# Kernel optimization log

Hardware: AMD Instinct MI355X
Metric: run time of the kernel (lower is better)

Reference implementation:

```python
import jax, jax.numpy as jnp
import numpy as np

N_NODES = 100000
N_EDGES = 3200000
IN_F = 128
HEADS = 8
OUT_C = 2  # GATConv out_channels hardcoded to 2 in the source
NEG_SLOPE = 0.2  # PyG GATConv default leaky_relu slope


def setup_inputs() -> dict:
    key = jax.random.key(0)
    ks = jax.random.split(key, 9)
    x = jax.random.normal(ks[0], (N_NODES, IN_F), dtype=jnp.float32)
    edge_index = jax.random.randint(ks[1], (2, N_EDGES), 0, N_NODES, dtype=jnp.int64)
    edge_attr = jax.random.uniform(ks[2], (N_EDGES, 1), dtype=jnp.float32)
    s = 1.0 / np.sqrt(IN_F)
    W = jax.random.normal(ks[3], (IN_F, HEADS * OUT_C), dtype=jnp.float32) * s
    att_src = jax.random.normal(ks[4], (HEADS, OUT_C), dtype=jnp.float32) * 0.5
    att_dst = jax.random.normal(ks[5], (HEADS, OUT_C), dtype=jnp.float32) * 0.5
    bias_gat = jnp.zeros((HEADS * OUT_C,), dtype=jnp.float32)
    W_fc = jax.random.normal(ks[6], (HEADS * OUT_C, 2), dtype=jnp.float32) * 0.25
    b_fc = jnp.zeros((2,), dtype=jnp.float32)
    return {"x": x, "edge_index": edge_index, "edge_attr": edge_attr,
            "W": W, "att_src": att_src, "att_dst": att_dst,
            "bias_gat": bias_gat, "W_fc": W_fc, "b_fc": b_fc}


def reference(x, edge_index, edge_attr, W, att_src, att_dst, bias_gat, W_fc, b_fc):
    # edge_attr is ignored: GATConv was built without edge_dim, matching the source.
    N = x.shape[0]
    # PyG GATConv adds self-loops by default
    loops = jnp.arange(N, dtype=edge_index.dtype)
    src = jnp.concatenate([edge_index[0], loops])  # [E']
    dst = jnp.concatenate([edge_index[1], loops])  # [E']

    h = (x @ W).reshape(N, HEADS, OUT_C)                 # [N,H,C]
    a_src = jnp.einsum('nhc,hc->nh', h, att_src)          # [N,H]
    a_dst = jnp.einsum('nhc,hc->nh', h, att_dst)          # [N,H]

    logits = jax.nn.leaky_relu(a_src[src] + a_dst[dst], negative_slope=NEG_SLOPE)  # [E',H]
    # segment softmax over edges grouped by destination node (self-loops ensure non-empty segments)
    seg_max = jax.ops.segment_max(logits, dst, num_segments=N)   # [N,H]
    p = jnp.exp(logits - seg_max[dst])                            # [E',H]
    seg_sum = jax.ops.segment_sum(p, dst, num_segments=N)         # [N,H]
    alpha = p / seg_sum[dst]                                      # [E',H]

    msg = alpha[:, :, None] * h[src]                              # [E',H,C]
    agg = jax.ops.segment_sum(msg, dst, num_segments=N)           # [N,H,C]
    gat_out = agg.reshape(N, HEADS * OUT_C) + bias_gat            # concat heads + bias
    return gat_out @ W_fc + b_fc                                  # [N,2]
```

## Files before the change

kernel.cpp:

```cpp
#include <hip/hip_runtime.h>
#include <hip/hip_fp16.h>

#define N_NODES 100000
#define IN_F 128
#define NF 16
#define HEADS 8
#define NEG_SLOPE 0.2f
#define LOG2E 1.44269504f

#define RB 256
#define LOG_RB 8
#define NB 391
#define SBITS 17
#define SMASK ((1u << SBITS) - 1)
#define BIN_C 4096
#define CAPB 9024


__device__ __forceinline__ void phase1_body(
    int pb, const float* __restrict__ x, const float* __restrict__ W,
    __half* __restrict__ rec, float* Ws)
{
    int t = threadIdx.x;
    for (int i = t; i < IN_F * NF; i += 512) Ws[i] = W[i];
    __syncthreads();

    int tid  = pb * 512 + t;
    int node = tid >> 3;
    int j    = tid & 7;
    if (node >= N_NODES) return;

    const float4* xr4 = (const float4*)(x + (size_t)node * IN_F);
    const float2* Wp  = (const float2*)Ws;

    float a0 = 0.f, b0 = 0.f, a1 = 0.f, b1 = 0.f;
    #pragma unroll 8
    for (int k4 = 0; k4 < IN_F / 4; ++k4) {
        float4 xv = xr4[k4];
        float2 w0 = Wp[(4 * k4 + 0) * 8 + j];
        float2 w1 = Wp[(4 * k4 + 1) * 8 + j];
        float2 w2 = Wp[(4 * k4 + 2) * 8 + j];
        float2 w3 = Wp[(4 * k4 + 3) * 8 + j];
        a0 = fmaf(xv.x, w0.x, a0); b0 = fmaf(xv.x, w0.y, b0);
        a1 = fmaf(xv.y, w1.x, a1); b1 = fmaf(xv.y, w1.y, b1);
        a0 = fmaf(xv.z, w2.x, a0); b0 = fmaf(xv.z, w2.y, b0);
        a1 = fmaf(xv.w, w3.x, a1); b1 = fmaf(xv.w, w3.y, b1);
    }
    __half2 hv = __floats2half2_rn(a0 + a1, b0 + b1);
    *(__half2*)(rec + (size_t)node * NF + 2 * j) = hv;
}

__global__ __launch_bounds__(512) void fused_p1_bin(
    const int* __restrict__ ei, int* __restrict__ bin_cursor,
    unsigned* __restrict__ bins,
    const float* __restrict__ x, const float* __restrict__ W,
    __half* __restrict__ rec, int E, int SB)
{
    __shared__ union {
        struct {
            unsigned staging[BIN_C];
            unsigned short bin16[BIN_C];
            int hist[NB], offs[NB], cur[NB], gbase[NB];
            int wsum[8], woff[8];
        } b;
        float Ws[IN_F * NF];
    } sm;

    int idx = blockIdx.x;
    bool is_bin = (idx % 3 == 0) && (idx / 3 < SB);
    if (!is_bin) {
        int cb = (idx + 2) / 3; if (cb > SB) cb = SB;
        phase1_body(idx - cb, x, W, rec, sm.Ws);
        return;
    }

    int t = threadIdx.x;
    int base = (idx / 3) * BIN_C;
    int n_valid = E - base;
    if (n_valid > BIN_C) n_valid = BIN_C;
    if (n_valid < 0) n_valid = 0;

    int es[8], ed[8];
    #pragma unroll
    for (int k = 0; k < 8; ++k) {
        int i = t + 512 * k;
        bool v = i < n_valid;
        es[k] = v ? ei[base + i] : 0;
        ed[k] = v ? ei[E + base + i] : -1;
    }

    if (t < NB) sm.b.hist[t] = 0;
    __syncthreads();

    #pragma unroll
    for (int k = 0; k < 8; ++k)
        if (ed[k] >= 0) atomicAdd(&sm.b.hist[ed[k] >> LOG_RB], 1);
    __syncthreads();

    int sum = (t < NB) ? sm.b.hist[t] : 0;
    int lane = t & 63, wid = t >> 6;
    int v = sum;
    #pragma unroll
    for (int o = 1; o < 64; o <<= 1) {
        int u = __shfl_up(v, o);
        if (lane >= o) v += u;
    }
    if (lane == 63) sm.b.wsum[wid] = v;
    __syncthreads();
    if (t == 0) { int r = 0; for (int w = 0; w < 8; ++w) { sm.b.woff[w] = r; r += sm.b.wsum[w]; } }
    __syncthreads();
    int run = sm.b.woff[wid] + v - sum;
    if (t < NB) { sm.b.offs[t] = run; sm.b.cur[t] = run; }
    __syncthreads();
    if (t < NB)
        sm.b.gbase[t] = sm.b.hist[t] ? atomicAdd(&bin_cursor[t], sm.b.hist[t]) : 0;
    __syncthreads();

    #pragma unroll
    for (int k = 0; k < 8; ++k) {
        if (ed[k] >= 0) {
            int b = ed[k] >> LOG_RB;
            int slot = atomicAdd(&sm.b.cur[b], 1);
            sm.b.staging[slot] = ((unsigned)(ed[k] & (RB - 1)) << SBITS) | (unsigned)es[k];
            sm.b.bin16[slot] = (unsigned short)b;
        }
    }
    __syncthreads();

    for (int i = t; i < n_valid; i += 512) {
        int b = sm.b.bin16[i];
        int pos = sm.b.gbase[b] + (i - sm.b.offs[b]);
        if (pos < CAPB) bins[(size_t)b * CAPB + pos] = sm.b.staging[i];
    }
}

__global__ __launch_bounds__(1024) void accum7_kernel(
    const unsigned* __restrict__ bins, const int* __restrict__ bin_cursor,
    const __half* __restrict__ rec,
    const float* __restrict__ att_src, const float* __restrict__ att_dst,
    const float* __restrict__ bias, const float* __restrict__ Wfc,
    const float* __restrict__ bfc, float* __restrict__ out)
{
    __shared__ unsigned staging[CAPB];
    __shared__ int hist[RB], offs[RB + 1], cur[RB];

    int t = threadIdx.x;
    int b = blockIdx.x;
    int node0 = b * RB;

    if (t < RB) hist[t] = 0;
    __syncthreads();

    int cnt = bin_cursor[b];
    if (cnt > CAPB) cnt = CAPB;
    const unsigned* seg = bins + (size_t)b * CAPB;

    unsigned rcache[9];
    int nk = 0;
    for (int i = t; i < cnt; i += 1024) rcache[nk++] = seg[i];

    for (int k = 0; k < nk; ++k)
        atomicAdd(&hist[rcache[k] >> SBITS], 1);
    __syncthreads();

    if (t < 64) {
        int h0 = hist[4 * t], h1 = hist[4 * t + 1];
        int h2 = hist[4 * t + 2], h3 = hist[4 * t + 3];
        int v = h0 + h1 + h2 + h3;
        int inc = v;
        #pragma unroll
        for (int o = 1; o < 64; o <<= 1) {
            int u = __shfl_up(inc, o);
            if (t >= o) inc += u;
        }
        int ex = inc - v;
        offs[4 * t] = ex;     cur[4 * t] = ex;     ex += h0;
        offs[4 * t + 1] = ex; cur[4 * t + 1] = ex; ex += h1;
        offs[4 * t + 2] = ex; cur[4 * t + 2] = ex; ex += h2;
        offs[4 * t + 3] = ex; cur[4 * t + 3] = ex;
        if (t == 63) offs[RB] = inc;
    }
    __syncthreads();

    for (int k = 0; k < nk; ++k) {
        unsigned r = rcache[k];
        int slot = atomicAdd(&cur[r >> SBITS], 1);
        staging[slot] = r & SMASK;
    }
    __syncthreads();

    int wv = t >> 6, lane = t & 63;
    int h_id = lane & 7, e_off = lane >> 3;

    float as0 = att_src[2 * h_id] * LOG2E, as1 = att_src[2 * h_id + 1] * LOG2E;
    float ad0 = att_dst[2 * h_id] * LOG2E, ad1 = att_dst[2 * h_id + 1] * LOG2E;
    float b0 = bias[2 * h_id], b1 = bias[2 * h_id + 1];
    float w00 = Wfc[(2 * h_id) * 2 + 0],     w01 = Wfc[(2 * h_id) * 2 + 1];
    float w10 = Wfc[(2 * h_id + 1) * 2 + 0], w11 = Wfc[(2 * h_id + 1) * 2 + 1];
    float c0 = bfc[0], c1 = bfc[1];

    for (int k = 0; k < RB / 16; ++k) {
        int ln = wv + 16 * k;
        int n = node0 + ln;
        if (n >= N_NODES) break;
        int st  = offs[ln];
        int deg = offs[ln + 1] - st;

        __half2 hn = *(const __half2*)(rec + (size_t)n * NF + 2 * h_id);
        float hn0 = __half2float(hn.x), hn1 = __half2float(hn.y);
        float adst_h = ad0 * hn0 + ad1 * hn1;

        float den = 0.f, num0 = 0.f, num1 = 0.f;
        float denB = 0.f, num0B = 0.f, num1B = 0.f;

        int i = e_off;
        for (; i + 8 < deg; i += 16) {
            int sA = staging[st + i];
            int sB = staging[st + i + 8];
            __half2 hsA = *(const __half2*)(rec + (size_t)sA * NF + 2 * h_id);
            __half2 hsB = *(const __half2*)(rec + (size_t)sB * NF + 2 * h_id);
            float hA0 = __half2float(hsA.x), hA1 = __half2float(hsA.y);
            float lA = fmaf(as0, hA0, fmaf(as1, hA1, adst_h));
            lA = lA > 0.f ? lA : NEG_SLOPE * lA;
            float pA = exp2f(lA);
            den += pA;
            num0 = fmaf(pA, hA0, num0);
            num1 = fmaf(pA, hA1, num1);
            float hB0 = __half2float(hsB.x), hB1 = __half2float(hsB.y);
            float lB = fmaf(as0, hB0, fmaf(as1, hB1, adst_h));
            lB = lB > 0.f ? lB : NEG_SLOPE * lB;
            float pB = exp2f(lB);
            denB += pB;
            num0B = fmaf(pB, hB0, num0B);
            num1B = fmaf(pB, hB1, num1B);
        }
        if (i < deg) {
            int s = staging[st + i];
            __half2 hs = *(const __half2*)(rec + (size_t)s * NF + 2 * h_id);
            float h0 = __half2float(hs.x), h1 = __half2float(hs.y);
            float l = fmaf(as0, h0, fmaf(as1, h1, adst_h));
            l = l > 0.f ? l : NEG_SLOPE * l;
            float p = exp2f(l);
            den += p;
            num0 = fmaf(p, h0, num0);
            num1 = fmaf(p, h1, num1);
        }
        den += denB; num0 += num0B; num1 += num1B;

        #pragma unroll
        for (int m = 8; m < 64; m <<= 1) {
            den  += __shfl_xor(den,  m);
            num0 += __shfl_xor(num0, m);
            num1 += __shfl_xor(num1, m);
        }
        {
            float l = fmaf(as0, hn0, fmaf(as1, hn1, adst_h));
            l = l > 0.f ? l : NEG_SLOPE * l;
            float p = exp2f(l);
            den += p;
            num0 = fmaf(p, hn0, num0);
            num1 = fmaf(p, hn1, num1);
        }
        float g0 = num0 / den + b0;
        float g1 = num1 / den + b1;
        float o0 = g0 * w00 + g1 * w10;
        float o1 = g0 * w01 + g1 * w11;
        #pragma unroll
        for (int m = 1; m < 8; m <<= 1) {
            o0 += __shfl_xor(o0, m);
            o1 += __shfl_xor(o1, m);
        }
        if (lane == 0) {
            float2 res = { o0 + c0, o1 + c1 };
            *(float2*)(out + (size_t)n * 2) = res;
        }
    }
}

extern "C" void kernel_launch(void* const* d_in, const int* in_sizes, int n_in,
                              void* d_out, int out_size, void* d_ws, size_t ws_size,
                              hipStream_t stream)
{
    const float* x       = (const float*)d_in[0];
    const int*   ei      = (const int*)d_in[1];
    const float* W       = (const float*)d_in[3];
    const float* att_src = (const float*)d_in[4];
    const float* att_dst = (const float*)d_in[5];
    const float* bias    = (const float*)d_in[6];
    const float* Wfc     = (const float*)d_in[7];
    const float* bfc     = (const float*)d_in[8];
    float*       out     = (float*)d_out;

    const int E  = in_sizes[1] / 2;
    const int SB = (E + BIN_C - 1) / BIN_C;
    const int PB = (N_NODES * 8 + 511) / 512;

    __half* rec        = (__half*)d_ws;
    int*    bin_cursor = (int*)((char*)d_ws + (size_t)N_NODES * NF * 2);
    size_t  bins_off   = (((size_t)((char*)bin_cursor - (char*)d_ws)) + NB * 4 + 4095) & ~(size_t)4095;
    unsigned* bins     = (unsigned*)((char*)d_ws + bins_off);

    hipMemsetAsync(bin_cursor, 0, NB * sizeof(int), stream);

    fused_p1_bin<<<SB + PB, 512, 0, stream>>>(
        ei, bin_cursor, bins, x, W, rec, E, SB);
    accum7_kernel<<<NB, 1024, 0, stream>>>(
        bins, bin_cursor, rec, att_src, att_dst, bias, Wfc, bfc, out);
}
```

Measured before the change: 204.8 us.

## Halve destination bin size and gather two heads per lane in accumulation

Bins now cover 128 destination nodes instead of 256, so there are twice as many bins and a smaller per-bin capacity. The accumulation kernel runs with 512 threads per block and launch bounds set for higher occupancy. Each lane now handles two heads using an 8-byte vector load, so four lanes cover a source row and sixteen edges are processed in parallel per wavefront. The aim is more resident blocks and fewer, wider gather loads, at the cost of more bins and global atomics in the binning pass. The smaller capacity also leaves less headroom against per-bin overflow.

```diff
diff --git a/kernel.cpp b/kernel.cpp
--- a/kernel.cpp
+++ b/kernel.cpp
@@ -8,13 +8,13 @@
 #define NEG_SLOPE 0.2f
 #define LOG2E 1.44269504f
 
-#define RB 256
-#define LOG_RB 8
-#define NB 391
+#define RB 128
+#define LOG_RB 7
+#define NB 782
 #define SBITS 17
 #define SMASK ((1u << SBITS) - 1)
 #define BIN_C 4096
-#define CAPB 9024
+#define CAPB 4608
 
 
 __device__ __forceinline__ void phase1_body(
@@ -89,7 +89,7 @@
         ed[k] = v ? ei[E + base + i] : -1;
     }
 
-    if (t < NB) sm.b.hist[t] = 0;
+    for (int i = t; i < NB; i += 512) sm.b.hist[i] = 0;
     __syncthreads();
 
     #pragma unroll
@@ -97,7 +97,10 @@
         if (ed[k] >= 0) atomicAdd(&sm.b.hist[ed[k] >> LOG_RB], 1);
     __syncthreads();
 
-    int sum = (t < NB) ? sm.b.hist[t] : 0;
+    int b0 = 2 * t, b1 = b0 + 1;
+    int h0 = (b0 < NB) ? sm.b.hist[b0] : 0;
+    int h1 = (b1 < NB) ? sm.b.hist[b1] : 0;
+    int sum = h0 + h1;
     int lane = t & 63, wid = t >> 6;
     int v = sum;
     #pragma unroll
@@ -110,31 +113,37 @@
     if (t == 0) { int r = 0; for (int w = 0; w < 8; ++w) { sm.b.woff[w] = r; r += sm.b.wsum[w]; } }
     __syncthreads();
     int run = sm.b.woff[wid] + v - sum;
-    if (t < NB) { sm.b.offs[t] = run; sm.b.cur[t] = run; }
-    __syncthreads();
-    if (t < NB)
-        sm.b.gbase[t] = sm.b.hist[t] ? atomicAdd(&bin_cursor[t], sm.b.hist[t]) : 0;
+    if (b0 < NB) { sm.b.offs[b0] = run; sm.b.cur[b0] = run; }
+    if (b1 < NB) { sm.b.offs[b1] = run + h0; sm.b.cur[b1] = run + h0; }
+    __syncthreads();
+    if (b0 < NB) sm.b.gbase[b0] = h0 ? atomicAdd(&bin_cursor[b0], h0) : 0;
+    if (b1 < NB) sm.b.gbase[b1] = h1 ? atomicAdd(&bin_cursor[b1], h1) : 0;
     __syncthreads();
 
     #pragma unroll
     for (int k = 0; k < 8; ++k) {
         if (ed[k] >= 0) {
-            int b = ed[k] >> LOG_RB;
-            int slot = atomicAdd(&sm.b.cur[b], 1);
+            int bb = ed[k] >> LOG_RB;
+            int slot = atomicAdd(&sm.b.cur[bb], 1);
             sm.b.staging[slot] = ((unsigned)(ed[k] & (RB - 1)) << SBITS) | (unsigned)es[k];
-            sm.b.bin16[slot] = (unsigned short)b;
+            sm.b.bin16[slot] = (unsigned short)bb;
         }
     }
     __syncthreads();
 
     for (int i = t; i < n_valid; i += 512) {
-        int b = sm.b.bin16[i];
-        int pos = sm.b.gbase[b] + (i - sm.b.offs[b]);
-        if (pos < CAPB) bins[(size_t)b * CAPB + pos] = sm.b.staging[i];
-    }
-}
-
-__global__ __launch_bounds__(1024) void accum7_kernel(
+        int bb = sm.b.bin16[i];
+        int pos = sm.b.gbase[bb] + (i - sm.b.offs[bb]);
+        if (pos < CAPB) bins[(size_t)bb * CAPB + pos] = sm.b.staging[i];
+    }
+}
+
+__device__ __forceinline__ float2 h2f2(unsigned u) {
+    __half2 h = *reinterpret_cast<__half2*>(&u);
+    return __half22float2(h);
+}
+
+__global__ __launch_bounds__(512, 8) void accum8_kernel(
     const unsigned* __restrict__ bins, const int* __restrict__ bin_cursor,
     const __half* __restrict__ rec,
     const float* __restrict__ att_src, const float* __restrict__ att_dst,
@@ -155,18 +164,21 @@
     if (cnt > CAPB) cnt = CAPB;
     const unsigned* seg = bins + (size_t)b * CAPB;
 
-    unsigned rcache[9];
-    int nk = 0;
-    for (int i = t; i < cnt; i += 1024) rcache[nk++] = seg[i];
-
-    for (int k = 0; k < nk; ++k)
-        atomicAdd(&hist[rcache[k] >> SBITS], 1);
+    unsigned rc[9];
+    #pragma unroll
+    for (int k = 0; k < 9; ++k) {
+        int i = t + 512 * k;
+        rc[k] = (i < cnt) ? seg[i] : 0xFFFFFFFFu;
+    }
+
+    #pragma unroll
+    for (int k = 0; k < 9; ++k)
+        if (rc[k] != 0xFFFFFFFFu) atomicAdd(&hist[rc[k] >> SBITS], 1);
     __syncthreads();
 
     if (t < 64) {
-        int h0 = hist[4 * t], h1 = hist[4 * t + 1];
-        int h2 = hist[4 * t + 2], h3 = hist[4 * t + 3];
-        int v = h0 + h1 + h2 + h3;
+        int h0 = hist[2 * t], h1 = hist[2 * t + 1];
+        int v = h0 + h1;
         int inc = v;
         #pragma unroll
         for (int o = 1; o < 64; o <<= 1) {
@@ -174,102 +186,124 @@
             if (t >= o) inc += u;
         }
         int ex = inc - v;
-        offs[4 * t] = ex;     cur[4 * t] = ex;     ex += h0;
-        offs[4 * t + 1] = ex; cur[4 * t + 1] = ex; ex += h1;
-        offs[4 * t + 2] = ex; cur[4 * t + 2] = ex; ex += h2;
-        offs[4 * t + 3] = ex; cur[4 * t + 3] = ex;
+        offs[2 * t] = ex;     cur[2 * t] = ex;     ex += h0;
+        offs[2 * t + 1] = ex; cur[2 * t + 1] = ex;
         if (t == 63) offs[RB] = inc;
     }
     __syncthreads();
 
-    for (int k = 0; k < nk; ++k) {
-        unsigned r = rcache[k];
-        int slot = atomicAdd(&cur[r >> SBITS], 1);
-        staging[slot] = r & SMASK;
+    #pragma unroll
+    for (int k = 0; k < 9; ++k) {
+        unsigned r = rc[k];
+        if (r != 0xFFFFFFFFu) {
+            int slot = atomicAdd(&cur[r >> SBITS], 1);
+            staging[slot] = r & SMASK;
+        }
     }
     __syncthreads();
 
     int wv = t >> 6, lane = t & 63;
-    int h_id = lane & 7, e_off = lane >> 3;
-
-    float as0 = att_src[2 * h_id] * LOG2E, as1 = att_src[2 * h_id + 1] * LOG2E;
-    float ad0 = att_dst[2 * h_id] * LOG2E, ad1 = att_dst[2 * h_id + 1] * LOG2E;
-    float b0 = bias[2 * h_id], b1 = bias[2 * h_id + 1];
-    float w00 = Wfc[(2 * h_id) * 2 + 0],     w01 = Wfc[(2 * h_id) * 2 + 1];
-    float w10 = Wfc[(2 * h_id + 1) * 2 + 0], w11 = Wfc[(2 * h_id + 1) * 2 + 1];
+    int part  = lane & 3;
+    int e_off = lane >> 2;
+
+    float asA0 = att_src[4 * part + 0] * LOG2E, asA1 = att_src[4 * part + 1] * LOG2E;
+    float asB0 = att_src[4 * part + 2] * LOG2E, asB1 = att_src[4 * part + 3] * LOG2E;
+    float adA0 = att_dst[4 * part + 0] * LOG2E, adA1 = att_dst[4 * part + 1] * LOG2E;
+    float adB0 = att_dst[4 * part + 2] * LOG2E, adB1 = att_dst[4 * part + 3] * LOG2E;
+    float bA0 = bias[4 * part + 0], bA1 = bias[4 * part + 1];
+    float bB0 = bias[4 * part + 2], bB1 = bias[4 * part + 3];
+    float wA00 = Wfc[(4 * part + 0) * 2 + 0], wA01 = Wfc[(4 * part + 0) * 2 + 1];
+    float wA10 = Wfc[(4 * part + 1) * 2 + 0], wA11 = Wfc[(4 * part + 1) * 2 + 1];
+    float wB00 = Wfc[(4 * part + 2) * 2 + 0], wB01 = Wfc[(4 * part + 2) * 2 + 1];
+    float wB10 = Wfc[(4 * part + 3) * 2 + 0], wB11 = Wfc[(4 * part + 3) * 2 + 1];
     float c0 = bfc[0], c1 = bfc[1];
 
-    for (int k = 0; k < RB / 16; ++k) {
-        int ln = wv + 16 * k;
+    const uint2* recq = (const uint2*)rec;
+
+    for (int k = 0; k < RB / 8; ++k) {
+        int ln = wv + 8 * k;
         int n = node0 + ln;
         if (n >= N_NODES) break;
         int st  = offs[ln];
         int deg = offs[ln + 1] - st;
 
-        __half2 hn = *(const __half2*)(rec + (size_t)n * NF + 2 * h_id);
-        float hn0 = __half2float(hn.x), hn1 = __half2float(hn.y);
-        float adst_h = ad0 * hn0 + ad1 * hn1;
-
-        float den = 0.f, num0 = 0.f, num1 = 0.f;
-        float denB = 0.f, num0B = 0.f, num1B = 0.f;
+        uint2 hq = recq[n * 4 + part];
+        float2 fnA = h2f2(hq.x), fnB = h2f2(hq.y);
+        float adstA = fmaf(adA0, fnA.x, adA1 * fnA.y);
+        float adstB = fmaf(adB0, fnB.x, adB1 * fnB.y);
+
+        float denA = 0.f, n0A = 0.f, n1A = 0.f;
+        float denB = 0.f, n0B = 0.f, n1B = 0.f;
 
         int i = e_off;
-        for (; i + 8 < deg; i += 16) {
-            int sA = staging[st + i];
-            int sB = staging[st + i + 8];
-            __half2 hsA = *(const __half2*)(rec + (size_t)sA * NF + 2 * h_id);
-            __half2 hsB = *(const __half2*)(rec + (size_t)sB * NF + 2 * h_id);
-            float hA0 = __half2float(hsA.x), hA1 = __half2float(hsA.y);
-            float lA = fmaf(as0, hA0, fmaf(as1, hA1, adst_h));
+        for (; i + 16 < deg; i += 32) {
+            int sX = staging[st + i];
+            int sY = staging[st + i + 16];
+            uint2 rX = recq[sX * 4 + part];
+            uint2 rY = recq[sY * 4 + part];
+            {
+                float2 xA = h2f2(rX.x), xB = h2f2(rX.y);
+                float lA = fmaf(asA0, xA.x, fmaf(asA1, xA.y, adstA));
+                lA = lA > 0.f ? lA : NEG_SLOPE * lA;
+                float pA = exp2f(lA);
+                denA += pA; n0A = fmaf(pA, xA.x, n0A); n1A = fmaf(pA, xA.y, n1A);
+                float lB = fmaf(asB0, xB.x, fmaf(asB1, xB.y, adstB));
+                lB = lB > 0.f ? lB : NEG_SLOPE * lB;
+                float pB = exp2f(lB);
+                denB += pB; n0B = fmaf(pB, xB.x, n0B); n1B = fmaf(pB, xB.y, n1B);
+            }
+            {
+                float2 xA = h2f2(rY.x), xB = h2f2(rY.y);
+                float lA = fmaf(asA0, xA.x, fmaf(asA1, xA.y, adstA));
+                lA = lA > 0.f ? lA : NEG_SLOPE * lA;
+                float pA = exp2f(lA);
+                denA += pA; n0A = fmaf(pA, xA.x, n0A); n1A = fmaf(pA, xA.y, n1A);
+                float lB = fmaf(asB0, xB.x, fmaf(asB1, xB.y, adstB));
+                lB = lB > 0.f ? lB : NEG_SLOPE * lB;
+                float pB = exp2f(lB);
+                denB += pB; n0B = fmaf(pB, xB.x, n0B); n1B = fmaf(pB, xB.y, n1B);
+            }
+        }
+        if (i < deg) {
+            int s = staging[st + i];
+            uint2 rX = recq[s * 4 + part];
+            float2 xA = h2f2(rX.x), xB = h2f2(rX.y);
+            float lA = fmaf(asA0, xA.x, fmaf(asA1, xA.y, adstA));
             lA = lA > 0.f ? lA : NEG_SLOPE * lA;
             float pA = exp2f(lA);
-            den += pA;
-            num0 = fmaf(pA, hA0, num0);
-            num1 = fmaf(pA, hA1, num1);
-            float hB0 = __half2float(hsB.x), hB1 = __half2float(hsB.y);
-            float lB = fmaf(as0, hB0, fmaf(as1, hB1, adst_h));
+            denA += pA; n0A = fmaf(pA, xA.x, n0A); n1A = fmaf(pA, xA.y, n1A);
+            float lB = fmaf(asB0, xB.x, fmaf(asB1, xB.y, adstB));
             lB = lB > 0.f ? lB : NEG_SLOPE * lB;
             float pB = exp2f(lB);
-            denB += pB;
-            num0B = fmaf(pB, hB0, num0B);
-            num1B = fmaf(pB, hB1, num1B);
-        }
-        if (i < deg) {
-            int s = staging[st + i];
-            __half2 hs = *(const __half2*)(rec + (size_t)s * NF + 2 * h_id);
-            float h0 = __half2float(hs.x), h1 = __half2float(hs.y);
-            float l = fmaf(as0, h0, fmaf(as1, h1, adst_h));
-            l = l > 0.f ? l : NEG_SLOPE * l;
-            float p = exp2f(l);
-            den += p;
-            num0 = fmaf(p, h0, num0);
-            num1 = fmaf(p, h1, num1);
-        }
-        den += denB; num0 += num0B; num1 += num1B;
+            denB += pB; n0B = fmaf(pB, xB.x, n0B); n1B = fmaf(pB, xB.y, n1B);
+        }
 
         #pragma unroll
-        for (int m = 8; m < 64; m <<= 1) {
-            den  += __shfl_xor(den,  m);
-            num0 += __shfl_xor(num0, m);
-            num1 += __shfl_xor(num1, m);
+        for (int m = 4; m < 64; m <<= 1) {
+            denA += __shfl_xor(denA, m);
+            n0A  += __shfl_xor(n0A, m);
+            n1A  += __shfl_xor(n1A, m);
+            denB += __shfl_xor(denB, m);
+            n0B  += __shfl_xor(n0B, m);
+            n1B  += __shfl_xor(n1B, m);
         }
         {
-            float l = fmaf(as0, hn0, fmaf(as1, hn1, adst_h));
-            l = l > 0.f ? l : NEG_SLOPE * l;
-            float p = exp2f(l);
-            den += p;
-            num0 = fmaf(p, hn0, num0);
-            num1 = fmaf(p, hn1, num1);
-        }
-        float g0 = num0 / den + b0;
-        float g1 = num1 / den + b1;
-        float o0 = g0 * w00 + g1 * w10;
-        float o1 = g0 * w01 + g1 * w11;
-        #pragma unroll
-        for (int m = 1; m < 8; m <<= 1) {
-            o0 += __shfl_xor(o0, m);
-            o1 += __shfl_xor(o1, m);
-        }
+            float lA = fmaf(asA0, fnA.x, fmaf(asA1, fnA.y, adstA));
+            lA = lA > 0.f ? lA : NEG_SLOPE * lA;
+            float pA = exp2f(lA);
+            denA += pA; n0A = fmaf(pA, fnA.x, n0A); n1A = fmaf(pA, fnA.y, n1A);
+            float lB = fmaf(asB0, fnB.x, fmaf(asB1, fnB.y, adstB));
+            lB = lB > 0.f ? lB : NEG_SLOPE * lB;
+            float pB = exp2f(lB);
+            denB += pB; n0B = fmaf(pB, fnB.x, n0B); n1B = fmaf(pB, fnB.y, n1B);
+        }
+        float iA = 1.f / denA, iB = 1.f / denB;
+        float gA0 = fmaf(n0A, iA, bA0), gA1 = fmaf(n1A, iA, bA1);
+        float gB0 = fmaf(n0B, iB, bB0), gB1 = fmaf(n1B, iB, bB1);
+        float o0 = gA0 * wA00 + gA1 * wA10 + gB0 * wB00 + gB1 * wB10;
+        float o1 = gA0 * wA01 + gA1 * wA11 + gB0 * wB01 + gB1 * wB11;
+        o0 += __shfl_xor(o0, 1); o0 += __shfl_xor(o0, 2);
+        o1 += __shfl_xor(o1, 1); o1 += __shfl_xor(o1, 2);
         if (lane == 0) {
             float2 res = { o0 + c0, o1 + c1 };
             *(float2*)(out + (size_t)n * 2) = res;
@@ -304,6 +338,6 @@
 
     fused_p1_bin<<<SB + PB, 512, 0, stream>>>(
         ei, bin_cursor, bins, x, W, rec, E, SB);
-    accum7_kernel<<<NB, 1024, 0, stream>>>(
+    accum8_kernel<<<NB, 512, 0, stream>>>(
         bins, bin_cursor, rec, att_src, att_dst, bias, Wfc, bfc, out);
 }
```

Measured after the change: 219.1 us. +7.0%, slower.
